# Performance work log

Measured on AMD Instinct MI355X. Metric: run time of the kernel, lower is better.

The kernel has to match this reference:

```python
import jax, jax.numpy as jnp
import numpy as np

B, C, H, W, K = 8, 256, 152, 152, 1024
MARGIN = 10.0
EPS = 1e-12  # F.normalize eps


def setup_inputs() -> dict:
    key = jax.random.key(0)
    k1, k2 = jax.random.split(key)
    output_id = jax.random.normal(k1, (B, C, H, W), dtype=jnp.float32)
    ind = jax.random.randint(k2, (B, K), 0, H * W)
    reg_mask = jnp.ones((B, K), dtype=jnp.int32)
    emb_scale = jnp.float32(10.0)
    return {"output_id": output_id, "ind": ind, "reg_mask": reg_mask, "emb_scale": emb_scale}


def reference(output_id, ind, reg_mask, emb_scale):
    b, c, h, w = output_id.shape
    # _tranpose_and_gather_feat: [B,C,H,W] -> [B,HW,C] -> gather ind -> [B,K,C]
    feat = output_id.transpose(0, 2, 3, 1).reshape(b, h * w, c)
    emb = jnp.take_along_axis(feat, ind[:, :, None], axis=1)  # [B,K,C]
    # emb_scale * F.normalize(emb)
    norm = jnp.maximum(jnp.linalg.norm(emb, axis=-1, keepdims=True), EPS)
    emb = emb_scale * (emb / norm)
    # pairwise euclidean distances per batch: [B,K,K]
    sq = jnp.sum(emb * emb, axis=-1)  # [B,K]
    d2 = sq[:, :, None] + sq[:, None, :] - 2.0 * jnp.einsum('bic,bjc->bij', emb, emb)
    dist = jnp.sqrt(jnp.maximum(d2, 0.0))
    # hardest negative: min over j != i, restricted to valid j
    valid = reg_mask > 0  # [B,K]
    big = jnp.float32(1e30)
    eye = jnp.eye(dist.shape[1], dtype=bool)[None]  # exclude self
    dist = jnp.where(eye | (~valid)[:, None, :], big, dist)
    neg_min = jnp.min(dist, axis=-1)  # [B,K]
    # HingeEmbeddingLoss with y = -1: mean over valid anchors of max(0, margin - d)
    hinge = jnp.maximum(MARGIN - neg_min, 0.0)
    vf = valid.astype(hinge.dtype)
    loss = jnp.sum(hinge * vf) / jnp.sum(vf)
    return loss
```

## Files before the change

### kernel.cpp

```cpp
#include <hip/hip_runtime.h>
#include <hip/hip_bf16.h>

#define Bz 8
#define Cc 256
#define HWp 23104
#define Kk 1024
#define BK (Bz*Kk)
#define MARGIN_F 10.0f
#define BIGF 1e30f
#define TILE 128
#define NBK 128

typedef __attribute__((ext_vector_type(8))) short bf16x8;
typedef __attribute__((ext_vector_type(4))) float f32x4;

__device__ __forceinline__ uint pk2(float a, float b) {
    return (uint)__hip_bfloat16_raw(__float2bfloat16(a)).x
         | ((uint)__hip_bfloat16_raw(__float2bfloat16(b)).x << 16);
}

__global__ __launch_bounds__(1024) void bucket_sort(
    const int* __restrict__ ind, uint* __restrict__ sorted,
    unsigned* __restrict__ neg)
{
    __shared__ uint cur[NBK];
    const int b = blockIdx.x, tid = threadIdx.x;
    if (tid < NBK) cur[tid] = 0;
    neg[b * Kk + tid] = __float_as_uint(BIGF);
    __syncthreads();
    int hw = ind[b * Kk + tid];
    int bk = hw >> 8;
    atomicAdd(&cur[bk], 1u);
    __syncthreads();
    if (tid == 0) {
        uint acc = 0;
        #pragma unroll
        for (int i = 0; i < NBK; ++i) { uint c = cur[i]; cur[i] = acc; acc += c; }
    }
    __syncthreads();
    uint slot = atomicAdd(&cur[bk], 1u);
    sorted[b * Kk + slot] = ((uint)hw << 10) | (uint)tid;
}

__global__ __launch_bounds__(256) void sorted_gather(
    const float* __restrict__ x, const uint* __restrict__ sorted,
    __hip_bfloat16* __restrict__ embr)
{
    const int kq = blockIdx.x, cg = blockIdx.y, b = blockIdx.z;
    const int c0 = cg * 32;
    const int t = threadIdx.x;
    const int kl = t >> 2, cq = t & 3;
    uint e = sorted[b * Kk + kq * 64 + kl];
    int hw = (int)(e >> 10), k = (int)(e & 1023u);
    const float* xp = x + (size_t)(b * Cc + c0 + cq * 8) * HWp + hw;
    float v[8];
    #pragma unroll
    for (int j = 0; j < 8; ++j) v[j] = xp[(size_t)j * HWp];
    uint4 o = make_uint4(pk2(v[0], v[1]), pk2(v[2], v[3]),
                         pk2(v[4], v[5]), pk2(v[6], v[7]));
    *(uint4*)((ushort*)embr + (size_t)(b * Kk + k) * Cc + c0 + cq * 8) = o;
}

__global__ __launch_bounds__(256) void rownorm(
    const __hip_bfloat16* __restrict__ embr, float* __restrict__ scl)
{
    int row  = blockIdx.x * 4 + (threadIdx.x >> 6);
    int lane = threadIdx.x & 63;
    uint2 v = *((const uint2*)((const ushort*)embr + (size_t)row * Cc) + lane);
    float f0 = __uint_as_float(v.x << 16);
    float f1 = __uint_as_float(v.x & 0xffff0000u);
    float f2 = __uint_as_float(v.y << 16);
    float f3 = __uint_as_float(v.y & 0xffff0000u);
    float s = f0*f0 + f1*f1 + f2*f2 + f3*f3;
    #pragma unroll
    for (int off = 32; off; off >>= 1) s += __shfl_xor(s, off);
    if (lane == 0)
        scl[row] = 10.0f / fmaxf(sqrtf(s), 1e-12f);
}

__global__ __launch_bounds__(256) void gram_mfma_min(
    const __hip_bfloat16* __restrict__ emb, const float* __restrict__ scl,
    const int* __restrict__ mask, unsigned* __restrict__ neg)
{
    __shared__ __align__(16) short As[TILE * 64];
    __shared__ __align__(16) short Bs[TILE * 64];
    int b  = blockIdx.z;
    int i0 = blockIdx.y * TILE;
    int j0 = blockIdx.x * TILE;
    int w  = threadIdx.x >> 6, l = threadIdx.x & 63;
    int wr = w >> 1, wc = w & 1;
    int lr = l & 15, lg = l >> 4;

    const short* E  = (const short*)emb + (size_t)b * Kk * Cc;
    const short* EA = E + (size_t)i0 * Cc;
    const short* EB = E + (size_t)j0 * Cc;

    const int lrow = l >> 3;
    const int lsub = (l & 7) ^ lrow;

    f32x4 acc[4][4] = {};
    for (int k0 = 0; k0 < Cc; k0 += 64) {
        #pragma unroll
        for (int q = 0; q < 4; ++q) {
            int t = w * 4 + q;
            int r = t * 8 + lrow;
            __builtin_amdgcn_global_load_lds(
                (const __attribute__((address_space(1))) void*)(EA + (size_t)r * Cc + k0 + lsub * 8),
                (__attribute__((address_space(3))) void*)&As[t * 512], 16, 0, 0);
            __builtin_amdgcn_global_load_lds(
                (const __attribute__((address_space(1))) void*)(EB + (size_t)r * Cc + k0 + lsub * 8),
                (__attribute__((address_space(3))) void*)&Bs[t * 512], 16, 0, 0);
        }
        __syncthreads();

        #pragma unroll
        for (int kk = 0; kk < 2; ++kk) {
            bf16x8 af[4], bf[4];
            #pragma unroll
            for (int f = 0; f < 4; ++f) {
                int ra = wr * 64 + f * 16 + lr;
                af[f] = *(const bf16x8*)&As[ra * 64 + (((kk * 4 + lg) ^ (ra & 7)) << 3)];
                int rb = wc * 64 + f * 16 + lr;
                bf[f] = *(const bf16x8*)&Bs[rb * 64 + (((kk * 4 + lg) ^ (rb & 7)) << 3)];
            }
            #pragma unroll
            for (int fi = 0; fi < 4; ++fi)
                #pragma unroll
                for (int fj = 0; fj < 4; ++fj)
                    acc[fi][fj] = __builtin_amdgcn_mfma_f32_16x16x32_bf16(
                                      af[fi], bf[fj], acc[fi][fj], 0, 0, 0);
        }
        __syncthreads();
    }

    const int* mb = mask + b * Kk;
    float cjv[4]; int jgv[4]; bool jva[4];
    #pragma unroll
    for (int fj = 0; fj < 4; ++fj) {
        int jg = j0 + wc*64 + fj*16 + lr;
        jgv[fj] = jg;
        cjv[fj] = scl[b * Kk + jg];
        jva[fj] = (mb[jg] != 0);
    }
    #pragma unroll
    for (int fi = 0; fi < 4; ++fi) {
        #pragma unroll
        for (int r = 0; r < 4; ++r) {
            int ig = i0 + wr*64 + fi*16 + 4*lg + r;
            float ci = scl[b * Kk + ig];
            float m = BIGF;
            #pragma unroll
            for (int fj = 0; fj < 4; ++fj) {
                float d2 = fmaxf(200.0f - 2.0f * ci * cjv[fj] * acc[fi][fj][r], 0.0f);
                bool ok = jva[fj] && (jgv[fj] != ig);
                m = ok ? fminf(m, d2) : m;
            }
            #pragma unroll
            for (int off = 1; off < 16; off <<= 1)
                m = fminf(m, __shfl_xor(m, off));
            if (lr == 0)
                atomicMin(&neg[b * Kk + ig], __float_as_uint(m));
        }
    }
}

__global__ __launch_bounds__(1024) void hinge_final(
    const unsigned* __restrict__ neg, const int* __restrict__ mask,
    float* __restrict__ out)
{
    float h = 0.f, v = 0.f;
    for (int i = threadIdx.x; i < BK; i += 1024) {
        if (mask[i] != 0) {
            float d = sqrtf(__uint_as_float(neg[i]));
            h += fmaxf(MARGIN_F - d, 0.f);
            v += 1.f;
        }
    }
    #pragma unroll
    for (int off = 32; off; off >>= 1) {
        h += __shfl_xor(h, off);
        v += __shfl_xor(v, off);
    }
    __shared__ float sh[16], sv[16];
    int w = threadIdx.x >> 6;
    if ((threadIdx.x & 63) == 0) { sh[w] = h; sv[w] = v; }
    __syncthreads();
    if (threadIdx.x == 0) {
        float H = 0.f, V = 0.f;
        #pragma unroll
        for (int i = 0; i < 16; ++i) { H += sh[i]; V += sv[i]; }
        out[0] = H / V;
    }
}

extern "C" void kernel_launch(void* const* d_in, const int* in_sizes, int n_in,
                              void* d_out, int out_size, void* d_ws, size_t ws_size,
                              hipStream_t stream) {
    const float* x    = (const float*)d_in[0];
    const int*   ind  = (const int*)d_in[1];
    const int*   mask = (const int*)d_in[2];
    float* out = (float*)d_out;

    __hip_bfloat16* embr = (__hip_bfloat16*)d_ws;
    float*    scl    = (float*)((char*)d_ws + (size_t)BK * Cc * sizeof(__hip_bfloat16));
    unsigned* neg    = (unsigned*)(scl + BK);
    uint*     sorted = (uint*)(neg + BK);

    bucket_sort<<<Bz, 1024, 0, stream>>>(ind, sorted, neg);
    dim3 g1(16, Cc / 32, Bz);
    sorted_gather<<<g1, 256, 0, stream>>>(x, sorted, embr);
    rownorm<<<BK / 4, 256, 0, stream>>>(embr, scl);
    dim3 g2(Kk / TILE, Kk / TILE, Bz);
    gram_mfma_min<<<g2, 256, 0, stream>>>(embr, scl, mask, neg);
    hinge_final<<<1, 1024, 0, stream>>>(neg, mask, out);
}
```

Baseline: 57.90 us.

## Fuse row norms and final hinge reduction into the Gram min kernel

Drops the separate rownorm and hinge_final launches. Each Gram tile block now computes the scale factors for its own 128 A rows and 128 B rows straight from bf16 embeddings into shared memory. A last-block-done counter lets the final block compute the hinge mean. This saves two kernel launches and the global round trip for the scales, at the cost of repeating norm work in every tile (8x redundant) and a serialized tail reduction done by one 256-thread block.

After: 89.62 us. +54.8%, slower.

```diff
diff --git a/kernel.cpp b/kernel.cpp
--- a/kernel.cpp
+++ b/kernel.cpp
@@ -21,12 +21,13 @@
 
 __global__ __launch_bounds__(1024) void bucket_sort(
     const int* __restrict__ ind, uint* __restrict__ sorted,
-    unsigned* __restrict__ neg)
+    unsigned* __restrict__ neg, unsigned* __restrict__ cnt)
 {
     __shared__ uint cur[NBK];
     const int b = blockIdx.x, tid = threadIdx.x;
     if (tid < NBK) cur[tid] = 0;
     neg[b * Kk + tid] = __float_as_uint(BIGF);
+    if (b == 0 && tid == 0) *cnt = 0u;
     __syncthreads();
     int hw = ind[b * Kk + tid];
     int bk = hw >> 8;
@@ -61,39 +62,45 @@
     *(uint4*)((ushort*)embr + (size_t)(b * Kk + k) * Cc + c0 + cq * 8) = o;
 }
 
-__global__ __launch_bounds__(256) void rownorm(
-    const __hip_bfloat16* __restrict__ embr, float* __restrict__ scl)
-{
-    int row  = blockIdx.x * 4 + (threadIdx.x >> 6);
-    int lane = threadIdx.x & 63;
-    uint2 v = *((const uint2*)((const ushort*)embr + (size_t)row * Cc) + lane);
-    float f0 = __uint_as_float(v.x << 16);
-    float f1 = __uint_as_float(v.x & 0xffff0000u);
-    float f2 = __uint_as_float(v.y << 16);
-    float f3 = __uint_as_float(v.y & 0xffff0000u);
-    float s = f0*f0 + f1*f1 + f2*f2 + f3*f3;
-    #pragma unroll
-    for (int off = 32; off; off >>= 1) s += __shfl_xor(s, off);
-    if (lane == 0)
-        scl[row] = 10.0f / fmaxf(sqrtf(s), 1e-12f);
-}
-
-__global__ __launch_bounds__(256) void gram_mfma_min(
-    const __hip_bfloat16* __restrict__ emb, const float* __restrict__ scl,
-    const int* __restrict__ mask, unsigned* __restrict__ neg)
+__global__ __launch_bounds__(256) void gram_min_hinge(
+    const __hip_bfloat16* __restrict__ emb, const int* __restrict__ mask,
+    unsigned* __restrict__ neg, unsigned* __restrict__ cnt,
+    float* __restrict__ out)
 {
     __shared__ __align__(16) short As[TILE * 64];
     __shared__ __align__(16) short Bs[TILE * 64];
+    __shared__ float scl_i[TILE], scl_j[TILE];
+    __shared__ uint lastFlag;
+
     int b  = blockIdx.z;
     int i0 = blockIdx.y * TILE;
     int j0 = blockIdx.x * TILE;
-    int w  = threadIdx.x >> 6, l = threadIdx.x & 63;
+    int tid = threadIdx.x;
+    int w  = tid >> 6, l = tid & 63;
     int wr = w >> 1, wc = w & 1;
     int lr = l & 15, lg = l >> 4;
 
     const short* E  = (const short*)emb + (size_t)b * Kk * Cc;
     const short* EA = E + (size_t)i0 * Cc;
     const short* EB = E + (size_t)j0 * Cc;
+
+    {
+        int m = tid >> 7;
+        int r = tid & 127;
+        const short* rp = (m ? EB : EA) + (size_t)r * Cc;
+        float s2 = 0.f;
+        #pragma unroll
+        for (int c = 0; c < 32; ++c) {
+            bf16x8 vv = *(const bf16x8*)(rp + c * 8);
+            #pragma unroll
+            for (int j = 0; j < 8; ++j) {
+                float f = __uint_as_float((uint)(ushort)vv[j] << 16);
+                s2 += f * f;
+            }
+        }
+        float sc = 10.0f / fmaxf(sqrtf(s2), 1e-12f);
+        if (m) scl_j[r] = sc; else scl_i[r] = sc;
+    }
 
     const int lrow = l >> 3;
     const int lsub = (l & 7) ^ lrow;
@@ -137,17 +144,18 @@
     float cjv[4]; int jgv[4]; bool jva[4];
     #pragma unroll
     for (int fj = 0; fj < 4; ++fj) {
-        int jg = j0 + wc*64 + fj*16 + lr;
-        jgv[fj] = jg;
-        cjv[fj] = scl[b * Kk + jg];
-        jva[fj] = (mb[jg] != 0);
+        int jl = wc * 64 + fj * 16 + lr;
+        jgv[fj] = j0 + jl;
+        cjv[fj] = scl_j[jl];
+        jva[fj] = (mb[j0 + jl] != 0);
     }
     #pragma unroll
     for (int fi = 0; fi < 4; ++fi) {
         #pragma unroll
         for (int r = 0; r < 4; ++r) {
-            int ig = i0 + wr*64 + fi*16 + 4*lg + r;
-            float ci = scl[b * Kk + ig];
+            int il = wr * 64 + fi * 16 + 4 * lg + r;
+            int ig = i0 + il;
+            float ci = scl_i[il];
             float m = BIGF;
             #pragma unroll
             for (int fj = 0; fj < 4; ++fj) {
@@ -162,34 +170,32 @@
                 atomicMin(&neg[b * Kk + ig], __float_as_uint(m));
         }
     }
-}
-
-__global__ __launch_bounds__(1024) void hinge_final(
-    const unsigned* __restrict__ neg, const int* __restrict__ mask,
-    float* __restrict__ out)
-{
-    float h = 0.f, v = 0.f;
-    for (int i = threadIdx.x; i < BK; i += 1024) {
-        if (mask[i] != 0) {
-            float d = sqrtf(__uint_as_float(neg[i]));
-            h += fmaxf(MARGIN_F - d, 0.f);
-            v += 1.f;
-        }
-    }
-    #pragma unroll
-    for (int off = 32; off; off >>= 1) {
-        h += __shfl_xor(h, off);
-        v += __shfl_xor(v, off);
-    }
-    __shared__ float sh[16], sv[16];
-    int w = threadIdx.x >> 6;
-    if ((threadIdx.x & 63) == 0) { sh[w] = h; sv[w] = v; }
-    __syncthreads();
-    if (threadIdx.x == 0) {
-        float H = 0.f, V = 0.f;
-        #pragma unroll
-        for (int i = 0; i < 16; ++i) { H += sh[i]; V += sv[i]; }
-        out[0] = H / V;
+
+    __threadfence();
+    if (tid == 0)
+        lastFlag = (atomicAdd(cnt, 1u) == 511u) ? 1u : 0u;
+    __syncthreads();
+    if (lastFlag) {
+        float h = 0.f, v = 0.f;
+        for (int i = tid; i < BK; i += 256) {
+            unsigned nb = __hip_atomic_load(&neg[i], __ATOMIC_RELAXED,
+                                            __HIP_MEMORY_SCOPE_AGENT);
+            if (mask[i] != 0) {
+                float d = sqrtf(__uint_as_float(nb));
+                h += fmaxf(MARGIN_F - d, 0.f);
+                v += 1.f;
+            }
+        }
+        #pragma unroll
+        for (int off = 32; off; off >>= 1) {
+            h += __shfl_xor(h, off);
+            v += __shfl_xor(v, off);
+        }
+        if (l == 0) { scl_i[w] = h; scl_i[4 + w] = v; }
+        __syncthreads();
+        if (tid == 0)
+            out[0] = (scl_i[0] + scl_i[1] + scl_i[2] + scl_i[3])
+                   / (scl_i[4] + scl_i[5] + scl_i[6] + scl_i[7]);
     }
 }
 
@@ -202,15 +208,13 @@
     float* out = (float*)d_out;
 
     __hip_bfloat16* embr = (__hip_bfloat16*)d_ws;
-    float*    scl    = (float*)((char*)d_ws + (size_t)BK * Cc * sizeof(__hip_bfloat16));
-    unsigned* neg    = (unsigned*)(scl + BK);
+    unsigned* neg    = (unsigned*)((char*)d_ws + (size_t)BK * Cc * sizeof(__hip_bfloat16));
     uint*     sorted = (uint*)(neg + BK);
-
-    bucket_sort<<<Bz, 1024, 0, stream>>>(ind, sorted, neg);
+    unsigned* cnt    = (unsigned*)(sorted + BK);
+
+    bucket_sort<<<Bz, 1024, 0, stream>>>(ind, sorted, neg, cnt);
     dim3 g1(16, Cc / 32, Bz);
     sorted_gather<<<g1, 256, 0, stream>>>(x, sorted, embr);
-    rownorm<<<BK / 4, 256, 0, stream>>>(embr, scl);
     dim3 g2(Kk / TILE, Kk / TILE, Bz);
-    gram_mfma_min<<<g2, 256, 0, stream>>>(embr, scl, mask, neg);
-    hinge_final<<<1, 1024, 0, stream>>>(neg, mask, out);
-}
+    gram_min_hinge<<<g2, 256, 0, stream>>>(embr, mask, neg, cnt, out);
+}
```
